# Kernel tuning notes

Hardware: AMD Instinct MI355X
Metric: run time of the kernel (lower is better)

Reference implementation:

```python
import jax, jax.numpy as jnp
import numpy as np

N_HEADS = 8
NODE_DIM, EDGE_DIM, TIME_DIM = 172, 172, 100
OUT_DIM = NODE_DIM + TIME_DIM  # 272, divisible by N_HEADS -> pad_dim = 0
HEAD_DIM = OUT_DIM // N_HEADS  # 34
KEY_DIM = NODE_DIM + EDGE_DIM + TIME_DIM  # 444
B, NBR = 4096, 64
LN_EPS = 1e-5


def setup_inputs() -> dict:
    key = jax.random.key(0)
    ks = jax.random.split(key, 12)
    s = 0.02
    return {
        "node_feat": jax.random.normal(ks[0], (B, NODE_DIM), jnp.float32),
        "time_feat": jax.random.normal(ks[1], (B, 1, TIME_DIM), jnp.float32),
        "edge_feat": jax.random.normal(ks[2], (B, NBR, EDGE_DIM), jnp.float32),
        "nbr_node_feat": jax.random.normal(ks[3], (B, NBR, NODE_DIM), jnp.float32),
        "nbr_time_feat": jax.random.normal(ks[4], (B, NBR, TIME_DIM), jnp.float32),
        "nbr_mask": jax.random.randint(ks[5], (B, NBR), 0, 2, jnp.int32),
        "W_Q": jax.random.normal(ks[6], (OUT_DIM, OUT_DIM), jnp.float32) * s,
        "W_KV": jax.random.normal(ks[7], (2 * OUT_DIM, KEY_DIM), jnp.float32) * s,
        "W_O": jax.random.normal(ks[8], (OUT_DIM, OUT_DIM), jnp.float32) * s,
        "b_O": jax.random.normal(ks[9], (OUT_DIM,), jnp.float32) * s,
        "ln_gamma": jnp.ones((OUT_DIM,), jnp.float32),
        "ln_beta": jnp.zeros((OUT_DIM,), jnp.float32),
    }


def reference(node_feat, time_feat, edge_feat, nbr_node_feat, nbr_time_feat,
              nbr_mask, W_Q, W_KV, W_O, b_O, ln_gamma, ln_beta):
    # Query/residual: concat node + time features -> (B, out_dim) (L=1 squeezed)
    R = jnp.concatenate([node_feat, time_feat[:, 0, :]], axis=-1)  # (B, D)
    Q = R @ W_Q.T  # (B, D)
    # Keys/values from neighbors
    Z_in = jnp.concatenate([nbr_node_feat, edge_feat, nbr_time_feat], axis=-1)  # (B,N,key_dim)
    Z = jnp.einsum('bnk,dk->bnd', Z_in, W_KV)  # (B, N, 2D)
    K, V = Z[..., :OUT_DIM], Z[..., OUT_DIM:]
    # Split heads
    Qh = Q.reshape(B, N_HEADS, HEAD_DIM)              # (B,H,d)
    Kh = K.reshape(B, NBR, N_HEADS, HEAD_DIM)         # (B,N,H,d)
    Vh = V.reshape(B, NBR, N_HEADS, HEAD_DIM)
    # Single-query attention scores: (B,H,N)
    scores = jnp.einsum('bhd,bnhd->bhn', Qh, Kh) * (HEAD_DIM ** -0.5)
    pad = (nbr_mask == 0)[:, None, :]  # (B,1,N)
    scores = jnp.where(pad, jnp.float32(-1e10), scores)
    A = jax.nn.softmax(scores, axis=-1)  # dropout is identity in eval / p=0
    O = jnp.einsum('bhn,bnhd->bhd', A, Vh).reshape(B, OUT_DIM)
    out = O @ W_O.T + b_O
    # Residual + LayerNorm
    x = out + R
    mu = jnp.mean(x, axis=-1, keepdims=True)
    var = jnp.mean(jnp.square(x - mu), axis=-1, keepdims=True)
    return (x - mu) * jax.lax.rsqrt(var + LN_EPS) * ln_gamma + ln_beta
```

## Files before the change

### kernel.cpp

```cpp
#include <hip/hip_runtime.h>
#include <hip/hip_bf16.h>
#include <string.h>

#define NROWS    4096
#define NBR      64
#define NODE_DIM 172
#define EDGE_DIM 172
#define TIME_DIM 100
#define OUT_DIM  272
#define KEY_DIM  444
#define KPAD     448
#define QK_PAD   320
#define N_HEADS  8
#define HEAD_DIM 34

typedef __attribute__((ext_vector_type(8))) short short8_t;
typedef __attribute__((ext_vector_type(4))) float f32x4;

__device__ inline short f2b(float x) {
  unsigned u = __builtin_bit_cast(unsigned, x);
  unsigned r = (u + 0x7fffu + ((u >> 16) & 1u)) >> 16;
  return (short)r;
}

__device__ inline unsigned pk2(float lo, float hi) {
  __hip_bfloat162 h = __float22bfloat162_rn(make_float2(lo, hi));
  unsigned u;
  memcpy(&u, &h, 4);
  return u;
}

template<int ROWS, int KP, int K0>
__device__ inline void pad_rows(char* A, int t) {
  constexpr int NC8 = (KP - K0) / 4;
  constexpr int LPR = 512 / ROWS;
  int r = t / LPR;
  int j = t % LPR;
  char* Arow = A + r * (2 * KP);
  int swz = (r & 7) << 4;
  uint2 zz; zz.x = 0; zz.y = 0;
  for (int c8 = j; c8 < NC8; c8 += LPR)
    *(uint2*)(Arow + ((2 * K0 + 8 * c8) ^ swz)) = zz;
}

template<int MT, int KP, int NKK>
__device__ inline void gemm_tile(const short* __restrict__ Wrow, const char* A,
                                 int lr, int lk, f32x4* acc) {
#pragma unroll
  for (int kk = 0; kk < NKK; ++kk) {
    short8_t bfrag = *(const short8_t*)(Wrow + lr * KP + kk * 32 + lk * 8);
#pragma unroll
    for (int mt = 0; mt < MT; ++mt) {
      short8_t afrag = *(const short8_t*)(A + (mt * 16 + lr) * (2 * KP) +
                                          ((kk * 64 + lk * 16) ^ ((lr & 7) << 4)));
      acc[mt] = __builtin_amdgcn_mfma_f32_16x16x32_bf16(afrag, bfrag, acc[mt], 0, 0, 0);
    }
  }
}

__global__ void convert_w(const float* __restrict__ Wkv, const float* __restrict__ Wq,
                          const float* __restrict__ Wo, short* __restrict__ wq_b,
                          short* __restrict__ wo_b, short* __restrict__ wkt,
                          short* __restrict__ wvh) {
  int i = blockIdx.x * 256 + threadIdx.x;
  if (i < OUT_DIM * QK_PAD) {
    int r = i / QK_PAD, c = i - r * QK_PAD;
    wq_b[i] = (c < OUT_DIM) ? f2b(Wq[r * OUT_DIM + c]) : (short)0;
    wo_b[i] = (c < OUT_DIM) ? f2b(Wo[r * OUT_DIM + c]) : (short)0;
  }
  if (i < N_HEADS * 448 * 64) {
    int h = i / 28672;
    int rem = i - h * 28672;
    int n = rem >> 6, d = rem & 63;
    wkt[i] = (n < KEY_DIM && d < HEAD_DIM) ? f2b(Wkv[(h * HEAD_DIM + d) * KEY_DIM + n])
                                           : (short)0;
  }
  if (i < N_HEADS * 48 * 448) {
    int h = i / 21504;
    int rem = i - h * 21504;
    int cp = rem / 448, k = rem - cp * 448;
    wvh[i] = (cp < HEAD_DIM && k < KEY_DIM)
                 ? f2b(Wkv[(OUT_DIM + h * HEAD_DIM + cp) * KEY_DIM + k])
                 : (short)0;
  }
}

__global__ __launch_bounds__(512) void q_qt(const float* __restrict__ node_feat,
                                            const float* __restrict__ time_feat,
                                            const short* __restrict__ Wq,
                                            const short* __restrict__ Wkt,
                                            short* __restrict__ Qtg) {
  __shared__ char Rlds[16 * 640];
  __shared__ char Qp[16 * 1024];
  int rb = blockIdx.x * 16, t = threadIdx.x;
  {
    int r = t >> 5, j = t & 31;
    const float4* pn = (const float4*)(node_feat + (size_t)(rb + r) * NODE_DIM);
    const float4* pt = (const float4*)(time_feat + (size_t)(rb + r) * TIME_DIM);
    float4 vn[2], vt4;
    int in_[2], it_;
#pragma unroll
    for (int i = 0; i < 2; ++i) { int f = j + 32 * i; in_[i] = f > 42 ? 42 : f; vn[i] = pn[in_[i]]; }
    it_ = j > 24 ? 24 : j; vt4 = pt[it_];
    char* Arow = Rlds + r * 640;
    int swz = (r & 7) << 4;
#pragma unroll
    for (int i = 0; i < 2; ++i) {
      uint2 w; w.x = pk2(vn[i].x, vn[i].y); w.y = pk2(vn[i].z, vn[i].w);
      *(uint2*)(Arow + ((8 * in_[i]) ^ swz)) = w;
    }
    {
      uint2 w; w.x = pk2(vt4.x, vt4.y); w.y = pk2(vt4.z, vt4.w);
      *(uint2*)(Arow + ((344 + 8 * it_) ^ swz)) = w;
    }
    if (j < 12) { uint2 zz; zz.x = 0; zz.y = 0; *(uint2*)(Arow + ((544 + 8 * j) ^ swz)) = zz; }
  }
  {
    uint4 zz; zz.x = 0; zz.y = 0; zz.z = 0; zz.w = 0;
    for (int i = t; i < 1024; i += 512) ((uint4*)Qp)[i] = zz;
  }
  __syncthreads();
  int wave = t >> 6, lane = t & 63, lr = lane & 15, lk = lane >> 4;
  f32x4 z = {0.f, 0.f, 0.f, 0.f};

  for (int nt = wave; nt < 17; nt += 8) {
    int nb = nt * 16;
    f32x4 acc[1] = {z};
    gemm_tile<1, QK_PAD, QK_PAD / 32>(Wq + nb * QK_PAD, Rlds, lr, lk, acc);
    int c = nb + lr;
    int h = c / HEAD_DIM, d = c - h * HEAD_DIM;
#pragma unroll
    for (int e = 0; e < 4; ++e) {
      int r = lk * 4 + e;
      *(short*)(Qp + r * 1024 + h * 128 + ((2 * d) ^ ((r & 7) << 4))) = f2b(acc[0][e]);
    }
  }
  __syncthreads();

  int h = wave;
  const short* Wh = Wkt + h * 28672;
  for (int nt = 0; nt < 28; ++nt) {
    f32x4 acc = z;
#pragma unroll
    for (int kk = 0; kk < 2; ++kk) {
      short8_t bfrag = *(const short8_t*)(Wh + (nt * 16 + lr) * 64 + kk * 32 + lk * 8);
      short8_t afrag = *(const short8_t*)(Qp + lr * 1024 + h * 128 +
                                          ((kk * 64 + lk * 16) ^ ((lr & 7) << 4)));
      acc = __builtin_amdgcn_mfma_f32_16x16x32_bf16(afrag, bfrag, acc, 0, 0, 0);
    }
#pragma unroll
    for (int e = 0; e < 4; ++e)
      Qtg[(size_t)(rb + lk * 4 + e) * 3584 + h * 448 + nt * 16 + lr] =
          f2b(acc[e] * 0.17149858514250882f);
  }
}

__global__ __launch_bounds__(256) void attn5(const float* __restrict__ nbr_node,
                                             const float* __restrict__ edge_feat,
                                             const float* __restrict__ nbr_time,
                                             const int* __restrict__ nbr_mask,
                                             const short* __restrict__ Qtg,
                                             short* __restrict__ Yh2) {
  __shared__ char Zc[32 * 896];
  __shared__ float Spart[2][32][8];
  __shared__ char Pb[16 * 64];
  __shared__ float Mh[8], Lh[8], Fh[8];
  int b = blockIdx.x;
  int t = threadIdx.x;
  int wave = t >> 6, lane = t & 63, lr = lane & 15, lk = lane >> 4;
  f32x4 z = {0.f, 0.f, 0.f, 0.f};
  f32x4 accY[7] = {z, z, z, z, z, z, z};

  for (int ch = 0; ch < 2; ++ch) {
    int n0 = ch * 32;
    {
      int r = t >> 3, j = t & 7;
      const float4* pn = (const float4*)(nbr_node + ((size_t)b * NBR + n0 + r) * NODE_DIM);
      const float4* pe = (const float4*)(edge_feat + ((size_t)b * NBR + n0 + r) * EDGE_DIM);
      const float4* pt = (const float4*)(nbr_time + ((size_t)b * NBR + n0 + r) * TIME_DIM);
      float4 vn[6], ve[6], vt4[4];
      int in_[6], it_[4];
#pragma unroll
      for (int i = 0; i < 6; ++i) { int f = j + 8 * i; in_[i] = f > 42 ? 42 : f; vn[i] = pn[in_[i]]; }
#pragma unroll
      for (int i = 0; i < 6; ++i) ve[i] = pe[in_[i]];
#pragma unroll
      for (int i = 0; i < 4; ++i) { int f = j + 8 * i; it_[i] = f > 24 ? 24 : f; vt4[i] = pt[it_[i]]; }
      char* Arow = Zc + r * 896;
      int swz = (r & 7) << 4;
#pragma unroll
      for (int i = 0; i < 6; ++i) {
        uint2 w; w.x = pk2(vn[i].x, vn[i].y); w.y = pk2(vn[i].z, vn[i].w);
        *(uint2*)(Arow + ((8 * in_[i]) ^ swz)) = w;
      }
#pragma unroll
      for (int i = 0; i < 6; ++i) {
        uint2 w; w.x = pk2(ve[i].x, ve[i].y); w.y = pk2(ve[i].z, ve[i].w);
        *(uint2*)(Arow + ((344 + 8 * in_[i]) ^ swz)) = w;
      }
#pragma unroll
      for (int i = 0; i < 4; ++i) {
        uint2 w; w.x = pk2(vt4[i].x, vt4[i].y); w.y = pk2(vt4[i].z, vt4[i].w);
        *(uint2*)(Arow + ((688 + 8 * it_[i]) ^ swz)) = w;
      }
      if (j == 0) { uint2 zz; zz.x = 0; zz.y = 0; *(uint2*)(Arow + (888 ^ swz)) = zz; }
    }
    __syncthreads();

    {
      int nt = wave & 1, kh = wave >> 1;
      f32x4 acc = z;
      const short* qrow = Qtg + (size_t)b * 3584 + (lr & 7) * 448;
      const char* zbase = Zc + (nt * 16 + lr) * 896;
      int swz = (lr & 7) << 4;
#pragma unroll
      for (int k7 = 0; k7 < 7; ++k7) {
        int ke = (kh * 7 + k7) * 32 + lk * 8;
        short8_t a = *(const short8_t*)(qrow + ke);
        short8_t bb = *(const short8_t*)(zbase + ((2 * ke) ^ swz));
        acc = __builtin_amdgcn_mfma_f32_16x16x32_bf16(a, bb, acc, 0, 0, 0);
      }
#pragma unroll
      for (int e = 0; e < 4; ++e) {
        int h = lk * 4 + e;
        if (h < 8) Spart[kh][nt * 16 + lr][h] = acc[e];
      }
    }
    __syncthreads();

    {
      int h = wave * 2 + (lane >> 5);
      int n = lane & 31;
      float s = Spart[0][n][h] + Spart[1][n][h];
      if (nbr_mask[(size_t)b * NBR + n0 + n] == 0) s = -1e10f;
      float m = s;
#pragma unroll
      for (int off = 16; off >= 1; off >>= 1) m = fmaxf(m, __shfl_xor(m, off));
      float mp = (ch == 0) ? -3e38f : Mh[h];
      float mn = fmaxf(mp, m);
      float e = __expf(s - mn);
      float sum = e;
#pragma unroll
      for (int off = 16; off >= 1; off >>= 1) sum += __shfl_xor(sum, off);
      float f = __expf(mp - mn);
      if (n == 0) {
        Lh[h] = (ch == 0 ? 0.f : Lh[h]) * f + sum;
        Mh[h] = mn;
        Fh[h] = f;
      }
      int off2 = (2 * n) ^ ((h & 3) << 4);
      *(short*)(Pb + h * 64 + off2) = f2b(e);
      *(short*)(Pb + (h + 8) * 64 + off2) = 0;
    }
    __syncthreads();

    {
      short8_t pa = *(const short8_t*)(Pb + lr * 64 + ((lk * 16) ^ ((lr & 3) << 4)));
      const char* zb_base = Zc + (lk * 8) * 896;
#pragma unroll
      for (int s7 = 0; s7 < 7; ++s7) {
        int vt = wave + 4 * s7;
#pragma unroll
        for (int e = 0; e < 4; ++e) accY[s7][e] *= Fh[(lk * 4 + e) & 7];
        int colb = 2 * (vt * 16 + lr);
        short8_t zb;
#pragma unroll
        for (int jx = 0; jx < 8; ++jx)
          zb[jx] = *(const short*)(zb_base + jx * 896 + (colb ^ (jx << 4)));
        accY[s7] = __builtin_amdgcn_mfma_f32_16x16x32_bf16(pa, zb, accY[s7], 0, 0, 0);
      }
    }
    __syncthreads();
  }

  if (lk < 2) {
    float inv[4];
#pragma unroll
    for (int e = 0; e < 4; ++e) inv[e] = 1.f / Lh[lk * 4 + e];
#pragma unroll
    for (int s7 = 0; s7 < 7; ++s7) {
      int vt = wave + 4 * s7;
      int k = vt * 16 + lr, kk2 = k >> 5, kp = k & 31;
#pragma unroll
      for (int e = 0; e < 4; ++e)
        Yh2[((size_t)((lk * 4 + e) * 14 + kk2) * 4096 + b) * 32 + kp] =
            f2b(accY[s7][e] * inv[e]);
    }
  }
}

__global__ __launch_bounds__(512) void out_ln2(const short* __restrict__ Yh2,
                                               const short* __restrict__ Wvh,
                                               const short* __restrict__ Wo,
                                               const float* __restrict__ bO,
                                               const float* __restrict__ node_feat,
                                               const float* __restrict__ time_feat,
                                               const float* __restrict__ gamma,
                                               const float* __restrict__ beta,
                                               float* __restrict__ out) {
  __shared__ char Alds[16 * 640];
  __shared__ float X[16 * 276];
  int rb = blockIdx.x * 16;
  int t = threadIdx.x;
  int wave = t >> 6, lane = t & 63, lr = lane & 15, lk = lane >> 4;
  pad_rows<16, QK_PAD, OUT_DIM>(Alds, t);
  f32x4 z = {0.f, 0.f, 0.f, 0.f};

  for (int p = wave; p < 24; p += 8) {
    int h = p / 3, nt = p - h * 3;
    f32x4 acc = z;
#pragma unroll
    for (int kk = 0; kk < 14; ++kk) {
      short8_t bfrag = *(const short8_t*)(Wvh + h * 21504 + (nt * 16 + lr) * 448 +
                                          kk * 32 + lk * 8);
      short8_t afrag = *(const short8_t*)(
          Yh2 + ((size_t)(h * 14 + kk) * 4096 + rb + lr) * 32 + lk * 8);
      acc = __builtin_amdgcn_mfma_f32_16x16x32_bf16(afrag, bfrag, acc, 0, 0, 0);
    }
    int cl = nt * 16 + lr;
    if (cl < HEAD_DIM) {
      int c = h * HEAD_DIM + cl;
#pragma unroll
      for (int e = 0; e < 4; ++e) {
        int r = lk * 4 + e;
        *(short*)(Alds + r * 640 + ((2 * c) ^ ((r & 7) << 4))) = f2b(acc[e]);
      }
    }
  }
  __syncthreads();

  for (int nt = wave; nt < 17; nt += 8) {
    int nb = nt * 16;
    f32x4 acc[1] = {z};
    gemm_tile<1, QK_PAD, QK_PAD / 32>(Wo + nb * QK_PAD, Alds, lr, lk, acc);
    int c = nb + lr;
    float bo = bO[c];
#pragma unroll
    for (int e = 0; e < 4; ++e) {
      int r = lk * 4 + e;
      int gr = rb + r;
      float Rv = (c < NODE_DIM) ? node_feat[(size_t)gr * NODE_DIM + c]
                                : time_feat[(size_t)gr * TIME_DIM + (c - NODE_DIM)];
      X[r * 276 + c] = acc[0][e] + bo + Rv;
    }
  }
  __syncthreads();

  int row = t >> 5, j = t & 31;
  float s1 = 0.f, s2 = 0.f;
  for (int c = j; c < OUT_DIM; c += 32) {
    float v = X[row * 276 + c];
    s1 += v; s2 += v * v;
  }
#pragma unroll
  for (int off = 16; off >= 1; off >>= 1) {
    s1 += __shfl_xor(s1, off);
    s2 += __shfl_xor(s2, off);
  }
  float mu = s1 * (1.f / OUT_DIM);
  float var = s2 * (1.f / OUT_DIM) - mu * mu;
  float inv = rsqrtf(fmaxf(var, 0.f) + 1e-5f);
  int gr = rb + row;
  for (int c = j; c < OUT_DIM; c += 32) {
    float v = X[row * 276 + c];
    out[(size_t)gr * OUT_DIM + c] = (v - mu) * inv * gamma[c] + beta[c];
  }
}

extern "C" void kernel_launch(void* const* d_in, const int* in_sizes, int n_in,
                              void* d_out, int out_size, void* d_ws, size_t ws_size,
                              hipStream_t stream) {
  const float* node_feat = (const float*)d_in[0];
  const float* time_feat = (const float*)d_in[1];
  const float* edge_feat = (const float*)d_in[2];
  const float* nbr_node  = (const float*)d_in[3];
  const float* nbr_time  = (const float*)d_in[4];
  const int*   nbr_mask  = (const int*)d_in[5];
  const float* W_Q   = (const float*)d_in[6];
  const float* W_KV  = (const float*)d_in[7];
  const float* W_O   = (const float*)d_in[8];
  const float* b_O   = (const float*)d_in[9];
  const float* gamma = (const float*)d_in[10];
  const float* beta  = (const float*)d_in[11];
  float* out = (float*)d_out;
  char* ws = (char*)d_ws;

  short* wq_b = (short*)(ws);
  short* wo_b = (short*)(ws + 174080);
  short* wvh  = (short*)(ws + 348160);
  short* wkt  = (short*)(ws + 692224);
  short* Qtg  = (short*)(ws + 1150976);
  short* Yh2  = (short*)(ws + 30511104);

  convert_w<<<896, 256, 0, stream>>>(W_KV, W_Q, W_O, wq_b, wo_b, wkt, wvh);
  q_qt<<<NROWS / 16, 512, 0, stream>>>(node_feat, time_feat, wq_b, wkt, Qtg);
  attn5<<<NROWS, 256, 0, stream>>>(nbr_node, edge_feat, nbr_time, nbr_mask, Qtg, Yh2);
  out_ln2<<<NROWS / 16, 512, 0, stream>>>(Yh2, wvh, wo_b, b_O, node_feat, time_feat,
                                          gamma, beta, out);
}
```

Before: 202.9 us.

## Double-buffer neighbor features via async global-to-LDS loads in persistent attention blocks

The attention kernel now runs 256 blocks of 512 threads, each processing 16 batch rows in 32 half-chunks. It uses global_load_lds to prefetch the next chunk's raw fp32 neighbor, edge and time rows into a second LDS buffer while the current one is computed. The fp32-to-bf16 conversion moves from staging into the MFMA operand fetch. The key dimension is re-padded per segment (480), so weight layouts, Qt and Yh2 strides change throughout the pipeline. The aim is to hide global load latency and remove register staging. The cost is doubled LDS (about 120KB per block), one resident block per CU, and repeated conversion work in the score and value passes.

```diff
diff --git a/kernel.cpp b/kernel.cpp
--- a/kernel.cpp
+++ b/kernel.cpp
@@ -9,13 +9,14 @@
 #define TIME_DIM 100
 #define OUT_DIM  272
 #define KEY_DIM  444
-#define KPAD     448
 #define QK_PAD   320
 #define N_HEADS  8
 #define HEAD_DIM 34
+#define KP3      480
 
 typedef __attribute__((ext_vector_type(8))) short short8_t;
 typedef __attribute__((ext_vector_type(4))) float f32x4;
+typedef __attribute__((ext_vector_type(4))) unsigned uintx4;
 
 __device__ inline short f2b(float x) {
   unsigned u = __builtin_bit_cast(unsigned, x);
@@ -28,6 +29,12 @@
   unsigned u;
   memcpy(&u, &h, 4);
   return u;
+}
+
+typedef const __attribute__((address_space(1))) void gv_t;
+typedef __attribute__((address_space(3))) void lv_t;
+__device__ inline void gld16(const void* g, void* l) {
+  __builtin_amdgcn_global_load_lds((gv_t*)g, (lv_t*)l, 16, 0, 0);
 }
 
 template<int ROWS, int KP, int K0>
@@ -58,6 +65,12 @@
   }
 }
 
+__device__ inline int kmap(int kp, bool& valid) {
+  if (kp < 176) { valid = kp < 172; return kp; }
+  if (kp < 352) { valid = kp < 348; return kp - 4; }
+  valid = kp < 452; return kp - 8;
+}
+
 __global__ void convert_w(const float* __restrict__ Wkv, const float* __restrict__ Wq,
                           const float* __restrict__ Wo, short* __restrict__ wq_b,
                           short* __restrict__ wo_b, short* __restrict__ wkt,
@@ -68,19 +81,20 @@
     wq_b[i] = (c < OUT_DIM) ? f2b(Wq[r * OUT_DIM + c]) : (short)0;
     wo_b[i] = (c < OUT_DIM) ? f2b(Wo[r * OUT_DIM + c]) : (short)0;
   }
-  if (i < N_HEADS * 448 * 64) {
-    int h = i / 28672;
-    int rem = i - h * 28672;
-    int n = rem >> 6, d = rem & 63;
-    wkt[i] = (n < KEY_DIM && d < HEAD_DIM) ? f2b(Wkv[(h * HEAD_DIM + d) * KEY_DIM + n])
-                                           : (short)0;
-  }
-  if (i < N_HEADS * 48 * 448) {
-    int h = i / 21504;
-    int rem = i - h * 21504;
-    int cp = rem / 448, k = rem - cp * 448;
-    wvh[i] = (cp < HEAD_DIM && k < KEY_DIM)
-                 ? f2b(Wkv[(OUT_DIM + h * HEAD_DIM + cp) * KEY_DIM + k])
+  if (i < N_HEADS * KP3 * 64) {
+    int h = i / (KP3 * 64);
+    int rem = i - h * (KP3 * 64);
+    int np = rem >> 6, d = rem & 63;
+    bool v; int kn = kmap(np, v);
+    wkt[i] = (v && d < HEAD_DIM) ? f2b(Wkv[(h * HEAD_DIM + d) * KEY_DIM + kn]) : (short)0;
+  }
+  if (i < N_HEADS * 48 * KP3) {
+    int h = i / (48 * KP3);
+    int rem = i - h * (48 * KP3);
+    int cp = rem / KP3, kp = rem - cp * KP3;
+    bool v; int kn = kmap(kp, v);
+    wvh[i] = (v && cp < HEAD_DIM)
+                 ? f2b(Wkv[(OUT_DIM + h * HEAD_DIM + cp) * KEY_DIM + kn])
                  : (short)0;
   }
 }
@@ -138,8 +152,8 @@
   __syncthreads();
 
   int h = wave;
-  const short* Wh = Wkt + h * 28672;
-  for (int nt = 0; nt < 28; ++nt) {
+  const short* Wh = Wkt + h * (KP3 * 64);
+  for (int nt = 0; nt < 30; ++nt) {
     f32x4 acc = z;
 #pragma unroll
     for (int kk = 0; kk < 2; ++kk) {
@@ -150,101 +164,114 @@
     }
 #pragma unroll
     for (int e = 0; e < 4; ++e)
-      Qtg[(size_t)(rb + lk * 4 + e) * 3584 + h * 448 + nt * 16 + lr] =
+      Qtg[(size_t)(rb + lk * 4 + e) * (8 * KP3) + h * KP3 + nt * 16 + lr] =
           f2b(acc[e] * 0.17149858514250882f);
   }
 }
 
-__global__ __launch_bounds__(256) void attn5(const float* __restrict__ nbr_node,
+__device__ inline void stage_issue(const float* __restrict__ nn,
+                                   const float* __restrict__ ef,
+                                   const float* __restrict__ tf,
+                                   int b, int half, char* buf, int wave, int lane) {
+  size_t rowbase = (size_t)b * NBR + half * 32;
+  for (int q = wave; q < 22; q += 8) {
+    int F = q * 1024 + lane * 16;
+    int row = (int)((unsigned)F / 704u);
+    int col = F - row * 704;
+    col = col > 672 ? 672 : col;
+    gld16((const char*)nn + (rowbase + row) * 688 + col, buf + q * 1024);
+  }
+  for (int q = wave; q < 22; q += 8) {
+    int F = q * 1024 + lane * 16;
+    int row = (int)((unsigned)F / 704u);
+    int col = F - row * 704;
+    col = col > 672 ? 672 : col;
+    gld16((const char*)ef + (rowbase + row) * 688 + col, buf + 22528 + q * 1024);
+  }
+  for (int q = wave; q < 16; q += 8) {
+    int F = q * 1024 + lane * 16;
+    int row = F >> 9;
+    int col = F & 511;
+    col = col > 384 ? 384 : col;
+    gld16((const char*)tf + (rowbase + row) * 400 + col, buf + 45056 + q * 1024);
+  }
+}
+
+__global__ __launch_bounds__(512) void attn6(const float* __restrict__ nbr_node,
                                              const float* __restrict__ edge_feat,
                                              const float* __restrict__ nbr_time,
                                              const int* __restrict__ nbr_mask,
                                              const short* __restrict__ Qtg,
                                              short* __restrict__ Yh2) {
-  __shared__ char Zc[32 * 896];
-  __shared__ float Spart[2][32][8];
+  __shared__ char Zb[2][61440];
+  __shared__ float Spart[4][32][8];
   __shared__ char Pb[16 * 64];
   __shared__ float Mh[8], Lh[8], Fh[8];
-  int b = blockIdx.x;
   int t = threadIdx.x;
   int wave = t >> 6, lane = t & 63, lr = lane & 15, lk = lane >> 4;
   f32x4 z = {0.f, 0.f, 0.f, 0.f};
-  f32x4 accY[7] = {z, z, z, z, z, z, z};
-
-  for (int ch = 0; ch < 2; ++ch) {
-    int n0 = ch * 32;
+  f32x4 accY[4] = {z, z, z, z};
+  int bbase = blockIdx.x * 16;
+
+  stage_issue(nbr_node, edge_feat, nbr_time, bbase, 0, Zb[0], wave, lane);
+  __syncthreads();
+
+  for (int ci = 0; ci < 32; ++ci) {
+    int b = bbase + (ci >> 1);
+    int half = ci & 1;
+    char* cur = Zb[ci & 1];
+    if (ci + 1 < 32)
+      stage_issue(nbr_node, edge_feat, nbr_time, bbase + ((ci + 1) >> 1), (ci + 1) & 1,
+                  Zb[(ci + 1) & 1], wave, lane);
+
     {
-      int r = t >> 3, j = t & 7;
-      const float4* pn = (const float4*)(nbr_node + ((size_t)b * NBR + n0 + r) * NODE_DIM);
-      const float4* pe = (const float4*)(edge_feat + ((size_t)b * NBR + n0 + r) * EDGE_DIM);
-      const float4* pt = (const float4*)(nbr_time + ((size_t)b * NBR + n0 + r) * TIME_DIM);
-      float4 vn[6], ve[6], vt4[4];
-      int in_[6], it_[4];
-#pragma unroll
-      for (int i = 0; i < 6; ++i) { int f = j + 8 * i; in_[i] = f > 42 ? 42 : f; vn[i] = pn[in_[i]]; }
-#pragma unroll
-      for (int i = 0; i < 6; ++i) ve[i] = pe[in_[i]];
-#pragma unroll
-      for (int i = 0; i < 4; ++i) { int f = j + 8 * i; it_[i] = f > 24 ? 24 : f; vt4[i] = pt[it_[i]]; }
-      char* Arow = Zc + r * 896;
-      int swz = (r & 7) << 4;
-#pragma unroll
-      for (int i = 0; i < 6; ++i) {
-        uint2 w; w.x = pk2(vn[i].x, vn[i].y); w.y = pk2(vn[i].z, vn[i].w);
-        *(uint2*)(Arow + ((8 * in_[i]) ^ swz)) = w;
-      }
-#pragma unroll
-      for (int i = 0; i < 6; ++i) {
-        uint2 w; w.x = pk2(ve[i].x, ve[i].y); w.y = pk2(ve[i].z, ve[i].w);
-        *(uint2*)(Arow + ((344 + 8 * in_[i]) ^ swz)) = w;
-      }
-#pragma unroll
-      for (int i = 0; i < 4; ++i) {
-        uint2 w; w.x = pk2(vt4[i].x, vt4[i].y); w.y = pk2(vt4[i].z, vt4[i].w);
-        *(uint2*)(Arow + ((688 + 8 * it_[i]) ^ swz)) = w;
-      }
-      if (j == 0) { uint2 zz; zz.x = 0; zz.y = 0; *(uint2*)(Arow + (888 ^ swz)) = zz; }
-    }
-    __syncthreads();
-
-    {
-      int nt = wave & 1, kh = wave >> 1;
+      int ntl = wave & 1, kh = wave >> 1;
       f32x4 acc = z;
-      const short* qrow = Qtg + (size_t)b * 3584 + (lr & 7) * 448;
-      const char* zbase = Zc + (nt * 16 + lr) * 896;
-      int swz = (lr & 7) << 4;
-#pragma unroll
-      for (int k7 = 0; k7 < 7; ++k7) {
-        int ke = (kh * 7 + k7) * 32 + lk * 8;
-        short8_t a = *(const short8_t*)(qrow + ke);
-        short8_t bb = *(const short8_t*)(zbase + ((2 * ke) ^ swz));
-        acc = __builtin_amdgcn_mfma_f32_16x16x32_bf16(a, bb, acc, 0, 0, 0);
+      const short* qrow = Qtg + (size_t)b * (8 * KP3) + (lr & 7) * KP3;
+      int r = ntl * 16 + lr;
+#pragma unroll
+      for (int k7 = 0; k7 < 4; ++k7) {
+        int kt = kh * 4 + k7;
+        if (kt < 15) {
+          int ke = kt * 32 + lk * 8;
+          const char* zrow; int cb;
+          if (ke < 176)      { zrow = cur + r * 704;         cb = 4 * ke; }
+          else if (ke < 352) { zrow = cur + 22528 + r * 704; cb = 4 * (ke - 176); }
+          else               { zrow = cur + 45056 + r * 512; cb = 4 * (ke - 352); }
+          float4 f0 = *(const float4*)(zrow + cb);
+          float4 f1 = *(const float4*)(zrow + cb + 16);
+          uintx4 pk;
+          pk[0] = pk2(f0.x, f0.y); pk[1] = pk2(f0.z, f0.w);
+          pk[2] = pk2(f1.x, f1.y); pk[3] = pk2(f1.z, f1.w);
+          short8_t bb = __builtin_bit_cast(short8_t, pk);
+          short8_t a = *(const short8_t*)(qrow + ke);
+          acc = __builtin_amdgcn_mfma_f32_16x16x32_bf16(a, bb, acc, 0, 0, 0);
+        }
       }
 #pragma unroll
       for (int e = 0; e < 4; ++e) {
         int h = lk * 4 + e;
-        if (h < 8) Spart[kh][nt * 16 + lr][h] = acc[e];
+        if (h < 8) Spart[kh][ntl * 16 + lr][h] = acc[e];
       }
     }
     __syncthreads();
 
     {
-      int h = wave * 2 + (lane >> 5);
-      int n = lane & 31;
-      float s = Spart[0][n][h] + Spart[1][n][h];
-      if (nbr_mask[(size_t)b * NBR + n0 + n] == 0) s = -1e10f;
+      int h = wave, n = lane & 31;
+      float s = Spart[0][n][h] + Spart[1][n][h] + Spart[2][n][h] + Spart[3][n][h];
+      if (nbr_mask[(size_t)b * NBR + half * 32 + n] == 0) s = -1e10f;
       float m = s;
 #pragma unroll
       for (int off = 16; off >= 1; off >>= 1) m = fmaxf(m, __shfl_xor(m, off));
-      float mp = (ch == 0) ? -3e38f : Mh[h];
+      float mp = (half == 0) ? -3e38f : Mh[h];
       float mn = fmaxf(mp, m);
       float e = __expf(s - mn);
       float sum = e;
 #pragma unroll
       for (int off = 16; off >= 1; off >>= 1) sum += __shfl_xor(sum, off);
       float f = __expf(mp - mn);
-      if (n == 0) {
-        Lh[h] = (ch == 0 ? 0.f : Lh[h]) * f + sum;
+      if (lane == 0) {
+        Lh[h] = (half ? Lh[h] : 0.f) * f + sum;
         Mh[h] = mn;
         Fh[h] = f;
       }
@@ -256,36 +283,51 @@
 
     {
       short8_t pa = *(const short8_t*)(Pb + lr * 64 + ((lk * 16) ^ ((lr & 3) << 4)));
-      const char* zb_base = Zc + (lk * 8) * 896;
-#pragma unroll
-      for (int s7 = 0; s7 < 7; ++s7) {
-        int vt = wave + 4 * s7;
-#pragma unroll
-        for (int e = 0; e < 4; ++e) accY[s7][e] *= Fh[(lk * 4 + e) & 7];
-        int colb = 2 * (vt * 16 + lr);
-        short8_t zb;
-#pragma unroll
-        for (int jx = 0; jx < 8; ++jx)
-          zb[jx] = *(const short*)(zb_base + jx * 896 + (colb ^ (jx << 4)));
-        accY[s7] = __builtin_amdgcn_mfma_f32_16x16x32_bf16(pa, zb, accY[s7], 0, 0, 0);
+#pragma unroll
+      for (int s7 = 0; s7 < 4; ++s7) {
+        int vt = wave + 8 * s7;
+        if (vt < 30) {
+          int kcol = vt * 16 + lr;
+          const char* zc; int strd;
+          if (kcol < 176)      { zc = cur + (lk * 8) * 704 + 4 * kcol;                strd = 704; }
+          else if (kcol < 352) { zc = cur + 22528 + (lk * 8) * 704 + 4 * (kcol - 176); strd = 704; }
+          else                 { zc = cur + 45056 + (lk * 8) * 512 + 4 * (kcol - 352); strd = 512; }
+          float zf0 = *(const float*)(zc);
+          float zf1 = *(const float*)(zc + strd);
+          float zf2 = *(const float*)(zc + 2 * strd);
+          float zf3 = *(const float*)(zc + 3 * strd);
+          float zf4 = *(const float*)(zc + 4 * strd);
+          float zf5 = *(const float*)(zc + 5 * strd);
+          float zf6 = *(const float*)(zc + 6 * strd);
+          float zf7 = *(const float*)(zc + 7 * strd);
+          uintx4 pk;
+          pk[0] = pk2(zf0, zf1); pk[1] = pk2(zf2, zf3);
+          pk[2] = pk2(zf4, zf5); pk[3] = pk2(zf6, zf7);
+          short8_t zb = __builtin_bit_cast(short8_t, pk);
+#pragma unroll
+          for (int e = 0; e < 4; ++e) accY[s7][e] *= Fh[(lk * 4 + e) & 7];
+          accY[s7] = __builtin_amdgcn_mfma_f32_16x16x32_bf16(pa, zb, accY[s7], 0, 0, 0);
+        }
+      }
+    }
+
+    if (half == 1 && lk < 2) {
+      float inv[4];
+#pragma unroll
+      for (int e = 0; e < 4; ++e) inv[e] = 1.f / Lh[lk * 4 + e];
+#pragma unroll
+      for (int s7 = 0; s7 < 4; ++s7) {
+        int vt = wave + 8 * s7;
+        if (vt < 30) {
+          int k = vt * 16 + lr, kk2 = k >> 5, kp = k & 31;
+#pragma unroll
+          for (int e = 0; e < 4; ++e)
+            Yh2[((size_t)((lk * 4 + e) * 15 + kk2) * 4096 + b) * 32 + kp] =
+                f2b(accY[s7][e] * inv[e]);
+        }
       }
     }
     __syncthreads();
-  }
-
-  if (lk < 2) {
-    float inv[4];
-#pragma unroll
-    for (int e = 0; e < 4; ++e) inv[e] = 1.f / Lh[lk * 4 + e];
-#pragma unroll
-    for (int s7 = 0; s7 < 7; ++s7) {
-      int vt = wave + 4 * s7;
-      int k = vt * 16 + lr, kk2 = k >> 5, kp = k & 31;
-#pragma unroll
-      for (int e = 0; e < 4; ++e)
-        Yh2[((size_t)((lk * 4 + e) * 14 + kk2) * 4096 + b) * 32 + kp] =
-            f2b(accY[s7][e] * inv[e]);
-    }
   }
 }
 
@@ -310,11 +352,11 @@
     int h = p / 3, nt = p - h * 3;
     f32x4 acc = z;
 #pragma unroll
-    for (int kk = 0; kk < 14; ++kk) {
-      short8_t bfrag = *(const short8_t*)(Wvh + h * 21504 + (nt * 16 + lr) * 448 +
+    for (int kk = 0; kk < 15; ++kk) {
+      short8_t bfrag = *(const short8_t*)(Wvh + h * (48 * KP3) + (nt * 16 + lr) * KP3 +
                                           kk * 32 + lk * 8);
       short8_t afrag = *(const short8_t*)(
-          Yh2 + ((size_t)(h * 14 + kk) * 4096 + rb + lr) * 32 + lk * 8);
+          Yh2 + ((size_t)(h * 15 + kk) * 4096 + rb + lr) * 32 + lk * 8);
       acc = __builtin_amdgcn_mfma_f32_16x16x32_bf16(afrag, bfrag, acc, 0, 0, 0);
     }
     int cl = nt * 16 + lr;
@@ -388,13 +430,13 @@
   short* wq_b = (short*)(ws);
   short* wo_b = (short*)(ws + 174080);
   short* wvh  = (short*)(ws + 348160);
-  short* wkt  = (short*)(ws + 692224);
-  short* Qtg  = (short*)(ws + 1150976);
-  short* Yh2  = (short*)(ws + 30511104);
-
-  convert_w<<<896, 256, 0, stream>>>(W_KV, W_Q, W_O, wq_b, wo_b, wkt, wvh);
+  short* wkt  = (short*)(ws + 716800);
+  short* Qtg  = (short*)(ws + 1208320);
+  short* Yh2  = (short*)(ws + 32665600);
+
+  convert_w<<<960, 256, 0, stream>>>(W_KV, W_Q, W_O, wq_b, wo_b, wkt, wvh);
   q_qt<<<NROWS / 16, 512, 0, stream>>>(node_feat, time_feat, wq_b, wkt, Qtg);
-  attn5<<<NROWS, 256, 0, stream>>>(nbr_node, edge_feat, nbr_time, nbr_mask, Qtg, Yh2);
+  attn6<<<256, 512, 0, stream>>>(nbr_node, edge_feat, nbr_time, nbr_mask, Qtg, Yh2);
   out_ln2<<<NROWS / 16, 512, 0, stream>>>(Yh2, wvh, wo_b, b_O, node_feat, time_feat,
                                           gamma, beta, out);
 }
```

Measured after the change: 223.1 us. 1.1x slower.

## Process all 64 neighbors in one pass with 512-thread attention blocks

Applied to the files above, without the earlier changes.

Replaces the two-chunk online-softmax attention kernel with a single pass. One 512-thread block stages all 64 neighbor rows in LDS, then computes scores, a plain softmax and the P·Z product. It also prefetches the Q fragments and the mask into registers before the feature load. This removes the per-chunk rescaling and several barriers, but doubles LDS use to about 57KB per block, which may limit how many blocks fit on each CU.

```diff
diff --git a/kernel.cpp b/kernel.cpp
--- a/kernel.cpp
+++ b/kernel.cpp
@@ -155,136 +155,120 @@
   }
 }
 
-__global__ __launch_bounds__(256) void attn5(const float* __restrict__ nbr_node,
+__global__ __launch_bounds__(512) void attn3(const float* __restrict__ nbr_node,
                                              const float* __restrict__ edge_feat,
                                              const float* __restrict__ nbr_time,
                                              const int* __restrict__ nbr_mask,
                                              const short* __restrict__ Qtg,
                                              short* __restrict__ Yh2) {
-  __shared__ char Zc[32 * 896];
-  __shared__ float Spart[2][32][8];
-  __shared__ char Pb[16 * 64];
-  __shared__ float Mh[8], Lh[8], Fh[8];
+  __shared__ char Alds[64 * 896];
+  __shared__ float Spart[2][64][8];
+  __shared__ char Pb[16 * 128];
   int b = blockIdx.x;
   int t = threadIdx.x;
   int wave = t >> 6, lane = t & 63, lr = lane & 15, lk = lane >> 4;
+
+  int ntw = wave & 3, kh = wave >> 2;
+  const short* qrow = Qtg + (size_t)b * 3584 + (lr & 7) * 448;
+  short8_t qpre[7];
+#pragma unroll
+  for (int k7 = 0; k7 < 7; ++k7)
+    qpre[k7] = *(const short8_t*)(qrow + (kh * 7 + k7) * 32 + lk * 8);
+  int mpre = nbr_mask[(size_t)b * NBR + lane];
+
+  {
+    int r = t >> 3, j = t & 7;
+    const float4* pn = (const float4*)(nbr_node + (size_t)b * NBR * NODE_DIM) + (size_t)r * 43;
+    const float4* pe = (const float4*)(edge_feat + (size_t)b * NBR * EDGE_DIM) + (size_t)r * 43;
+    const float4* pt = (const float4*)(nbr_time + (size_t)b * NBR * TIME_DIM) + (size_t)r * 25;
+    float4 vn[6], ve[6], vt4[4];
+    int in_[6], it_[4];
+#pragma unroll
+    for (int i = 0; i < 6; ++i) { int f = j + 8 * i; in_[i] = f > 42 ? 42 : f; vn[i] = pn[in_[i]]; }
+#pragma unroll
+    for (int i = 0; i < 6; ++i) { ve[i] = pe[in_[i]]; }
+#pragma unroll
+    for (int i = 0; i < 4; ++i) { int f = j + 8 * i; it_[i] = f > 24 ? 24 : f; vt4[i] = pt[it_[i]]; }
+    char* Arow = Alds + r * 896;
+    int swz = (r & 7) << 4;
+#pragma unroll
+    for (int i = 0; i < 6; ++i) {
+      uint2 w; w.x = pk2(vn[i].x, vn[i].y); w.y = pk2(vn[i].z, vn[i].w);
+      *(uint2*)(Arow + ((8 * in_[i]) ^ swz)) = w;
+    }
+#pragma unroll
+    for (int i = 0; i < 6; ++i) {
+      uint2 w; w.x = pk2(ve[i].x, ve[i].y); w.y = pk2(ve[i].z, ve[i].w);
+      *(uint2*)(Arow + ((344 + 8 * in_[i]) ^ swz)) = w;
+    }
+#pragma unroll
+    for (int i = 0; i < 4; ++i) {
+      uint2 w; w.x = pk2(vt4[i].x, vt4[i].y); w.y = pk2(vt4[i].z, vt4[i].w);
+      *(uint2*)(Arow + ((688 + 8 * it_[i]) ^ swz)) = w;
+    }
+    if (j == 0) { uint2 zz; zz.x = 0; zz.y = 0; *(uint2*)(Arow + (888 ^ swz)) = zz; }
+  }
+  __syncthreads();
+
   f32x4 z = {0.f, 0.f, 0.f, 0.f};
-  f32x4 accY[7] = {z, z, z, z, z, z, z};
-
-  for (int ch = 0; ch < 2; ++ch) {
-    int n0 = ch * 32;
-    {
-      int r = t >> 3, j = t & 7;
-      const float4* pn = (const float4*)(nbr_node + ((size_t)b * NBR + n0 + r) * NODE_DIM);
-      const float4* pe = (const float4*)(edge_feat + ((size_t)b * NBR + n0 + r) * EDGE_DIM);
-      const float4* pt = (const float4*)(nbr_time + ((size_t)b * NBR + n0 + r) * TIME_DIM);
-      float4 vn[6], ve[6], vt4[4];
-      int in_[6], it_[4];
-#pragma unroll
-      for (int i = 0; i < 6; ++i) { int f = j + 8 * i; in_[i] = f > 42 ? 42 : f; vn[i] = pn[in_[i]]; }
-#pragma unroll
-      for (int i = 0; i < 6; ++i) ve[i] = pe[in_[i]];
-#pragma unroll
-      for (int i = 0; i < 4; ++i) { int f = j + 8 * i; it_[i] = f > 24 ? 24 : f; vt4[i] = pt[it_[i]]; }
-      char* Arow = Zc + r * 896;
-      int swz = (r & 7) << 4;
-#pragma unroll
-      for (int i = 0; i < 6; ++i) {
-        uint2 w; w.x = pk2(vn[i].x, vn[i].y); w.y = pk2(vn[i].z, vn[i].w);
-        *(uint2*)(Arow + ((8 * in_[i]) ^ swz)) = w;
-      }
-#pragma unroll
-      for (int i = 0; i < 6; ++i) {
-        uint2 w; w.x = pk2(ve[i].x, ve[i].y); w.y = pk2(ve[i].z, ve[i].w);
-        *(uint2*)(Arow + ((344 + 8 * in_[i]) ^ swz)) = w;
-      }
-#pragma unroll
-      for (int i = 0; i < 4; ++i) {
-        uint2 w; w.x = pk2(vt4[i].x, vt4[i].y); w.y = pk2(vt4[i].z, vt4[i].w);
-        *(uint2*)(Arow + ((688 + 8 * it_[i]) ^ swz)) = w;
-      }
-      if (j == 0) { uint2 zz; zz.x = 0; zz.y = 0; *(uint2*)(Arow + (888 ^ swz)) = zz; }
-    }
-    __syncthreads();
-
-    {
-      int nt = wave & 1, kh = wave >> 1;
-      f32x4 acc = z;
-      const short* qrow = Qtg + (size_t)b * 3584 + (lr & 7) * 448;
-      const char* zbase = Zc + (nt * 16 + lr) * 896;
-      int swz = (lr & 7) << 4;
-#pragma unroll
-      for (int k7 = 0; k7 < 7; ++k7) {
-        int ke = (kh * 7 + k7) * 32 + lk * 8;
-        short8_t a = *(const short8_t*)(qrow + ke);
-        short8_t bb = *(const short8_t*)(zbase + ((2 * ke) ^ swz));
-        acc = __builtin_amdgcn_mfma_f32_16x16x32_bf16(a, bb, acc, 0, 0, 0);
-      }
+
+  {
+    f32x4 acc = z;
+    const char* zbase = Alds + (ntw * 16 + lr) * 896;
+    int swz = (lr & 7) << 4;
+#pragma unroll
+    for (int k7 = 0; k7 < 7; ++k7) {
+      int ke = (kh * 7 + k7) * 32 + lk * 8;
+      short8_t bbv = *(const short8_t*)(zbase + ((2 * ke) ^ swz));
+      acc = __builtin_amdgcn_mfma_f32_16x16x32_bf16(qpre[k7], bbv, acc, 0, 0, 0);
+    }
+#pragma unroll
+    for (int e = 0; e < 4; ++e) {
+      int h = lk * 4 + e;
+      if (h < 8) Spart[kh][ntw * 16 + lr][h] = acc[e];
+    }
+  }
+  __syncthreads();
+
+  {
+    int h = wave, n = lane;
+    float s = Spart[0][n][h] + Spart[1][n][h];
+    if (mpre == 0) s = -1e10f;
+    float m = s;
+#pragma unroll
+    for (int off = 32; off >= 1; off >>= 1) m = fmaxf(m, __shfl_xor(m, off));
+    float e = __expf(s - m);
+    float sum = e;
+#pragma unroll
+    for (int off = 32; off >= 1; off >>= 1) sum += __shfl_xor(sum, off);
+    int off2 = (2 * n) ^ ((h & 7) << 4);
+    *(short*)(Pb + h * 128 + off2) = f2b(e / sum);
+    *(short*)(Pb + (h + 8) * 128 + off2) = 0;
+  }
+  __syncthreads();
+
+  for (int vt = wave; vt < 28; vt += 8) {
+    int vb = vt * 16;
+    f32x4 acc = z;
+    int colb = 2 * (vb + lr);
+#pragma unroll
+    for (int kk = 0; kk < 2; ++kk) {
+      short8_t pa = *(const short8_t*)(Pb + lr * 128 +
+                                       ((kk * 64 + lk * 16) ^ ((lr & 7) << 4)));
+      const char* zb_base = Alds + (kk * 32 + lk * 8) * 896;
+      short8_t zb;
+#pragma unroll
+      for (int j = 0; j < 8; ++j)
+        zb[j] = *(const short*)(zb_base + j * 896 + (colb ^ (j << 4)));
+      acc = __builtin_amdgcn_mfma_f32_16x16x32_bf16(pa, zb, acc, 0, 0, 0);
+    }
+    if (lk < 2) {
+      int k = vb + lr, kk2 = k >> 5, kp = k & 31;
 #pragma unroll
       for (int e = 0; e < 4; ++e) {
         int h = lk * 4 + e;
-        if (h < 8) Spart[kh][nt * 16 + lr][h] = acc[e];
+        Yh2[((size_t)(h * 14 + kk2) * 4096 + b) * 32 + kp] = f2b(acc[e]);
       }
-    }
-    __syncthreads();
-
-    {
-      int h = wave * 2 + (lane >> 5);
-      int n = lane & 31;
-      float s = Spart[0][n][h] + Spart[1][n][h];
-      if (nbr_mask[(size_t)b * NBR + n0 + n] == 0) s = -1e10f;
-      float m = s;
-#pragma unroll
-      for (int off = 16; off >= 1; off >>= 1) m = fmaxf(m, __shfl_xor(m, off));
-      float mp = (ch == 0) ? -3e38f : Mh[h];
-      float mn = fmaxf(mp, m);
-      float e = __expf(s - mn);
-      float sum = e;
-#pragma unroll
-      for (int off = 16; off >= 1; off >>= 1) sum += __shfl_xor(sum, off);
-      float f = __expf(mp - mn);
-      if (n == 0) {
-        Lh[h] = (ch == 0 ? 0.f : Lh[h]) * f + sum;
-        Mh[h] = mn;
-        Fh[h] = f;
-      }
-      int off2 = (2 * n) ^ ((h & 3) << 4);
-      *(short*)(Pb + h * 64 + off2) = f2b(e);
-      *(short*)(Pb + (h + 8) * 64 + off2) = 0;
-    }
-    __syncthreads();
-
-    {
-      short8_t pa = *(const short8_t*)(Pb + lr * 64 + ((lk * 16) ^ ((lr & 3) << 4)));
-      const char* zb_base = Zc + (lk * 8) * 896;
-#pragma unroll
-      for (int s7 = 0; s7 < 7; ++s7) {
-        int vt = wave + 4 * s7;
-#pragma unroll
-        for (int e = 0; e < 4; ++e) accY[s7][e] *= Fh[(lk * 4 + e) & 7];
-        int colb = 2 * (vt * 16 + lr);
-        short8_t zb;
-#pragma unroll
-        for (int jx = 0; jx < 8; ++jx)
-          zb[jx] = *(const short*)(zb_base + jx * 896 + (colb ^ (jx << 4)));
-        accY[s7] = __builtin_amdgcn_mfma_f32_16x16x32_bf16(pa, zb, accY[s7], 0, 0, 0);
-      }
-    }
-    __syncthreads();
-  }
-
-  if (lk < 2) {
-    float inv[4];
-#pragma unroll
-    for (int e = 0; e < 4; ++e) inv[e] = 1.f / Lh[lk * 4 + e];
-#pragma unroll
-    for (int s7 = 0; s7 < 7; ++s7) {
-      int vt = wave + 4 * s7;
-      int k = vt * 16 + lr, kk2 = k >> 5, kp = k & 31;
-#pragma unroll
-      for (int e = 0; e < 4; ++e)
-        Yh2[((size_t)((lk * 4 + e) * 14 + kk2) * 4096 + b) * 32 + kp] =
-            f2b(accY[s7][e] * inv[e]);
     }
   }
 }
@@ -394,7 +378,7 @@
 
   convert_w<<<896, 256, 0, stream>>>(W_KV, W_Q, W_O, wq_b, wo_b, wkt, wvh);
   q_qt<<<NROWS / 16, 512, 0, stream>>>(node_feat, time_feat, wq_b, wkt, Qtg);
-  attn5<<<NROWS, 256, 0, stream>>>(nbr_node, edge_feat, nbr_time, nbr_mask, Qtg, Yh2);
+  attn3<<<NROWS, 512, 0, stream>>>(nbr_node, edge_feat, nbr_time, nbr_mask, Qtg, Yh2);
   out_ln2<<<NROWS / 16, 512, 0, stream>>>(Yh2, wvh, wo_b, b_O, node_feat, time_feat,
                                           gamma, beta, out);
 }
```

New measurement: 170.3 us. 1.19x faster.

## Make attention kernel persistent with double-buffered async global-to-LDS neighbor loads

Applied to the files above, without the earlier changes.

Replaces the one-block-per-row attention kernel with a 512-thread block that loops over 16 rows in 32-neighbor chunks. The next chunk's fp32 neighbor features and the precomputed Qt row are prefetched directly into LDS with global_load_lds while the current chunk is converted and processed. The Qt layout is also changed to a swizzled form so it can be staged into LDS. This aims to hide global memory latency and cut per-block launch overhead. The cost is a large LDS footprint (about 130KB), which limits occupancy to roughly one block per CU, and only 256 blocks are launched.

```diff
diff --git a/kernel.cpp b/kernel.cpp
--- a/kernel.cpp
+++ b/kernel.cpp
@@ -28,6 +28,18 @@
   unsigned u;
   memcpy(&u, &h, 4);
   return u;
+}
+
+typedef const __attribute__((address_space(1))) void gv_t;
+typedef __attribute__((address_space(3))) void lv_t;
+__device__ inline void gld16(const void* g, void* l) {
+  __builtin_amdgcn_global_load_lds((gv_t*)g, (lv_t*)l, 16, 0, 0);
+}
+
+__device__ inline void barrier_lgkm() {
+  asm volatile("s_waitcnt lgkmcnt(0)" ::: "memory");
+  __builtin_amdgcn_sched_barrier(0);
+  __builtin_amdgcn_s_barrier();
 }
 
 template<int ROWS, int KP, int K0>
@@ -149,102 +161,142 @@
       acc = __builtin_amdgcn_mfma_f32_16x16x32_bf16(afrag, bfrag, acc, 0, 0, 0);
     }
 #pragma unroll
-    for (int e = 0; e < 4; ++e)
-      Qtg[(size_t)(rb + lk * 4 + e) * 3584 + h * 448 + nt * 16 + lr] =
-          f2b(acc[e] * 0.17149858514250882f);
-  }
-}
-
-__global__ __launch_bounds__(256) void attn5(const float* __restrict__ nbr_node,
-                                             const float* __restrict__ edge_feat,
-                                             const float* __restrict__ nbr_time,
+    for (int e = 0; e < 4; ++e) {
+      int n = nt * 16 + lr;
+      *(short*)((char*)Qtg + (size_t)(rb + lk * 4 + e) * 7168 + h * 896 +
+                ((2 * n) ^ (h << 4))) = f2b(acc[e] * 0.17149858514250882f);
+    }
+  }
+}
+
+__device__ inline void stage_chunk(const float* __restrict__ nn,
+                                   const float* __restrict__ ef,
+                                   const float* __restrict__ tf,
+                                   const short* __restrict__ Qtg,
+                                   int b, int half, char* buf, char* qtslot, char* dump,
+                                   int wave, int lane) {
+  size_t row0 = (size_t)b * NBR + half * 32;
+  const char* nb = (const char*)(nn + row0 * NODE_DIM);
+  const char* eb = (const char*)(ef + row0 * EDGE_DIM);
+  const char* tb = (const char*)(tf + row0 * TIME_DIM);
+  const char* qb = (const char*)Qtg + (size_t)b * 7168;
+#pragma unroll
+  for (int i = 0; i < 8; ++i) {
+    int q = wave * 8 + i;
+    if (q < 22) {
+      int off = q * 1024 + lane * 16; if (off > 22000) off = 22000;
+      gld16(nb + off, buf + q * 1024);
+    } else if (q < 44) {
+      int off = (q - 22) * 1024 + lane * 16; if (off > 22000) off = 22000;
+      gld16(eb + off, buf + 22528 + (q - 22) * 1024);
+    } else if (q < 57) {
+      int off = (q - 44) * 1024 + lane * 16; if (off > 12784) off = 12784;
+      gld16(tb + off, buf + 45056 + (q - 44) * 1024);
+    } else {
+      int off = (q - 57) * 1024 + lane * 16;
+      gld16(qb + off, half == 0 ? (qtslot + (q - 57) * 1024) : dump);
+    }
+  }
+}
+
+__global__ __launch_bounds__(512) void attn7(const float* __restrict__ nn,
+                                             const float* __restrict__ ef,
+                                             const float* __restrict__ tf,
                                              const int* __restrict__ nbr_mask,
                                              const short* __restrict__ Qtg,
                                              short* __restrict__ Yh2) {
-  __shared__ char Zc[32 * 896];
-  __shared__ float Spart[2][32][8];
+  __shared__ char Zbuf[2][58368];
+  __shared__ char QtS[2][7168];
+  __shared__ char Dump[1024];
+  __shared__ float Spart[4][32][8];
   __shared__ char Pb[16 * 64];
   __shared__ float Mh[8], Lh[8], Fh[8];
-  int b = blockIdx.x;
+  __shared__ int Mlds[1024];
   int t = threadIdx.x;
   int wave = t >> 6, lane = t & 63, lr = lane & 15, lk = lane >> 4;
+  int bbase = blockIdx.x * 16;
   f32x4 z = {0.f, 0.f, 0.f, 0.f};
-  f32x4 accY[7] = {z, z, z, z, z, z, z};
-
-  for (int ch = 0; ch < 2; ++ch) {
-    int n0 = ch * 32;
+  f32x4 accY[4] = {z, z, z, z};
+
+  if (t < 256) ((int4*)Mlds)[t] = ((const int4*)(nbr_mask + (size_t)bbase * 64))[t];
+  stage_chunk(nn, ef, tf, Qtg, bbase, 0, Zbuf[0], QtS[0], Dump, wave, lane);
+
+  for (int ci = 0; ci < 32; ++ci) {
+    int b = bbase + (ci >> 1), half = ci & 1;
+    char* cur = Zbuf[ci & 1];
+
+    if (ci < 31) {
+      int b2 = bbase + ((ci + 1) >> 1);
+      stage_chunk(nn, ef, tf, Qtg, b2, (ci + 1) & 1, Zbuf[(ci + 1) & 1], QtS[b2 & 1],
+                  Dump, wave, lane);
+      asm volatile("s_waitcnt vmcnt(8) lgkmcnt(0)" ::: "memory");
+    } else {
+      asm volatile("s_waitcnt vmcnt(0) lgkmcnt(0)" ::: "memory");
+    }
+    __builtin_amdgcn_sched_barrier(0);
+    __builtin_amdgcn_s_barrier();
+
+    int r = t >> 4, j = t & 15;
+    f32x4 v[7];
+#pragma unroll
+    for (int i = 0; i < 7; ++i) {
+      int k = j * 4 + i * 64;
+      int off = (k < 172) ? (r * 688 + 4 * k)
+              : (k < 344) ? (22528 + r * 688 + 4 * (k - 172))
+                          : (45056 + r * 400 + 4 * (k - 344));
+      v[i] = *(const f32x4*)(cur + off);
+    }
+    if (j == 15) { v[6][0] = 0.f; v[6][1] = 0.f; v[6][2] = 0.f; v[6][3] = 0.f; }
+    barrier_lgkm();
     {
-      int r = t >> 3, j = t & 7;
-      const float4* pn = (const float4*)(nbr_node + ((size_t)b * NBR + n0 + r) * NODE_DIM);
-      const float4* pe = (const float4*)(edge_feat + ((size_t)b * NBR + n0 + r) * EDGE_DIM);
-      const float4* pt = (const float4*)(nbr_time + ((size_t)b * NBR + n0 + r) * TIME_DIM);
-      float4 vn[6], ve[6], vt4[4];
-      int in_[6], it_[4];
-#pragma unroll
-      for (int i = 0; i < 6; ++i) { int f = j + 8 * i; in_[i] = f > 42 ? 42 : f; vn[i] = pn[in_[i]]; }
-#pragma unroll
-      for (int i = 0; i < 6; ++i) ve[i] = pe[in_[i]];
-#pragma unroll
-      for (int i = 0; i < 4; ++i) { int f = j + 8 * i; it_[i] = f > 24 ? 24 : f; vt4[i] = pt[it_[i]]; }
-      char* Arow = Zc + r * 896;
+      char* Arow = cur + r * 896;
       int swz = (r & 7) << 4;
 #pragma unroll
-      for (int i = 0; i < 6; ++i) {
-        uint2 w; w.x = pk2(vn[i].x, vn[i].y); w.y = pk2(vn[i].z, vn[i].w);
-        *(uint2*)(Arow + ((8 * in_[i]) ^ swz)) = w;
-      }
-#pragma unroll
-      for (int i = 0; i < 6; ++i) {
-        uint2 w; w.x = pk2(ve[i].x, ve[i].y); w.y = pk2(ve[i].z, ve[i].w);
-        *(uint2*)(Arow + ((344 + 8 * in_[i]) ^ swz)) = w;
-      }
-#pragma unroll
-      for (int i = 0; i < 4; ++i) {
-        uint2 w; w.x = pk2(vt4[i].x, vt4[i].y); w.y = pk2(vt4[i].z, vt4[i].w);
-        *(uint2*)(Arow + ((688 + 8 * it_[i]) ^ swz)) = w;
-      }
-      if (j == 0) { uint2 zz; zz.x = 0; zz.y = 0; *(uint2*)(Arow + (888 ^ swz)) = zz; }
-    }
-    __syncthreads();
+      for (int i = 0; i < 7; ++i) {
+        uint2 w; w.x = pk2(v[i][0], v[i][1]); w.y = pk2(v[i][2], v[i][3]);
+        *(uint2*)(Arow + ((8 * j + 128 * i) ^ swz)) = w;
+      }
+    }
+    barrier_lgkm();
 
     {
-      int nt = wave & 1, kh = wave >> 1;
+      int ntl = wave & 1, kq = wave >> 1;
+      int tb0 = kq < 2 ? kq * 4 : 8 + (kq - 2) * 3;
+      int cnt = kq < 2 ? 4 : 3;
       f32x4 acc = z;
-      const short* qrow = Qtg + (size_t)b * 3584 + (lr & 7) * 448;
-      const char* zbase = Zc + (nt * 16 + lr) * 896;
+      const char* qbase = QtS[b & 1] + (lr & 7) * 896;
+      const char* zbase = cur + (ntl * 16 + lr) * 896;
       int swz = (lr & 7) << 4;
-#pragma unroll
-      for (int k7 = 0; k7 < 7; ++k7) {
-        int ke = (kh * 7 + k7) * 32 + lk * 8;
-        short8_t a = *(const short8_t*)(qrow + ke);
-        short8_t bb = *(const short8_t*)(zbase + ((2 * ke) ^ swz));
+      for (int it = 0; it < cnt; ++it) {
+        int keb = 2 * ((tb0 + it) * 32 + lk * 8);
+        short8_t a = *(const short8_t*)(qbase + (keb ^ swz));
+        short8_t bb = *(const short8_t*)(zbase + (keb ^ swz));
         acc = __builtin_amdgcn_mfma_f32_16x16x32_bf16(a, bb, acc, 0, 0, 0);
       }
 #pragma unroll
       for (int e = 0; e < 4; ++e) {
         int h = lk * 4 + e;
-        if (h < 8) Spart[kh][nt * 16 + lr][h] = acc[e];
-      }
-    }
-    __syncthreads();
+        if (h < 8) Spart[kq][ntl * 16 + lr][h] = acc[e];
+      }
+    }
+    barrier_lgkm();
 
     {
-      int h = wave * 2 + (lane >> 5);
-      int n = lane & 31;
-      float s = Spart[0][n][h] + Spart[1][n][h];
-      if (nbr_mask[(size_t)b * NBR + n0 + n] == 0) s = -1e10f;
+      int h = wave, n = lane & 31;
+      float s = Spart[0][n][h] + Spart[1][n][h] + Spart[2][n][h] + Spart[3][n][h];
+      if (Mlds[(ci >> 1) * 64 + half * 32 + n] == 0) s = -1e10f;
       float m = s;
 #pragma unroll
       for (int off = 16; off >= 1; off >>= 1) m = fmaxf(m, __shfl_xor(m, off));
-      float mp = (ch == 0) ? -3e38f : Mh[h];
+      float mp = (half == 0) ? -3e38f : Mh[h];
       float mn = fmaxf(mp, m);
       float e = __expf(s - mn);
       float sum = e;
 #pragma unroll
       for (int off = 16; off >= 1; off >>= 1) sum += __shfl_xor(sum, off);
       float f = __expf(mp - mn);
-      if (n == 0) {
-        Lh[h] = (ch == 0 ? 0.f : Lh[h]) * f + sum;
+      if (lane == 0) {
+        Lh[h] = (half ? Lh[h] : 0.f) * f + sum;
         Mh[h] = mn;
         Fh[h] = f;
       }
@@ -252,40 +304,43 @@
       *(short*)(Pb + h * 64 + off2) = f2b(e);
       *(short*)(Pb + (h + 8) * 64 + off2) = 0;
     }
-    __syncthreads();
+    barrier_lgkm();
 
     {
       short8_t pa = *(const short8_t*)(Pb + lr * 64 + ((lk * 16) ^ ((lr & 3) << 4)));
-      const char* zb_base = Zc + (lk * 8) * 896;
-#pragma unroll
-      for (int s7 = 0; s7 < 7; ++s7) {
-        int vt = wave + 4 * s7;
-#pragma unroll
-        for (int e = 0; e < 4; ++e) accY[s7][e] *= Fh[(lk * 4 + e) & 7];
-        int colb = 2 * (vt * 16 + lr);
-        short8_t zb;
-#pragma unroll
-        for (int jx = 0; jx < 8; ++jx)
-          zb[jx] = *(const short*)(zb_base + jx * 896 + (colb ^ (jx << 4)));
-        accY[s7] = __builtin_amdgcn_mfma_f32_16x16x32_bf16(pa, zb, accY[s7], 0, 0, 0);
-      }
-    }
-    __syncthreads();
-  }
-
-  if (lk < 2) {
-    float inv[4];
-#pragma unroll
-    for (int e = 0; e < 4; ++e) inv[e] = 1.f / Lh[lk * 4 + e];
-#pragma unroll
-    for (int s7 = 0; s7 < 7; ++s7) {
-      int vt = wave + 4 * s7;
-      int k = vt * 16 + lr, kk2 = k >> 5, kp = k & 31;
-#pragma unroll
-      for (int e = 0; e < 4; ++e)
-        Yh2[((size_t)((lk * 4 + e) * 14 + kk2) * 4096 + b) * 32 + kp] =
-            f2b(accY[s7][e] * inv[e]);
-    }
+#pragma unroll
+      for (int s7 = 0; s7 < 4; ++s7) {
+        int vt = wave + 8 * s7;
+        if (vt < 28) {
+          int colb = 2 * (vt * 16 + lr);
+          const char* zb_base = cur + (lk * 8) * 896;
+          short8_t zb;
+#pragma unroll
+          for (int jx = 0; jx < 8; ++jx)
+            zb[jx] = *(const short*)(zb_base + jx * 896 + (colb ^ (jx << 4)));
+#pragma unroll
+          for (int e = 0; e < 4; ++e) accY[s7][e] *= Fh[(lk * 4 + e) & 7];
+          accY[s7] = __builtin_amdgcn_mfma_f32_16x16x32_bf16(pa, zb, accY[s7], 0, 0, 0);
+        }
+      }
+      if (half == 1 && lk < 2) {
+        float inv[4];
+#pragma unroll
+        for (int e = 0; e < 4; ++e) inv[e] = 1.f / Lh[lk * 4 + e];
+#pragma unroll
+        for (int s7 = 0; s7 < 4; ++s7) {
+          int vt = wave + 8 * s7;
+          if (vt < 28) {
+            int k = vt * 16 + lr, kk2 = k >> 5, kp = k & 31;
+#pragma unroll
+            for (int e = 0; e < 4; ++e)
+              Yh2[((size_t)((lk * 4 + e) * 14 + kk2) * 4096 + b) * 32 + kp] =
+                  f2b(accY[s7][e] * inv[e]);
+          }
+        }
+      }
+    }
+    __builtin_amdgcn_s_barrier();
   }
 }
 
@@ -394,7 +449,7 @@
 
   convert_w<<<896, 256, 0, stream>>>(W_KV, W_Q, W_O, wq_b, wo_b, wkt, wvh);
   q_qt<<<NROWS / 16, 512, 0, stream>>>(node_feat, time_feat, wq_b, wkt, Qtg);
-  attn5<<<NROWS, 256, 0, stream>>>(nbr_node, edge_feat, nbr_time, nbr_mask, Qtg, Yh2);
+  attn7<<<256, 512, 0, stream>>>(nbr_node, edge_feat, nbr_time, nbr_mask, Qtg, Yh2);
   out_ln2<<<NROWS / 16, 512, 0, stream>>>(Yh2, wvh, wo_b, b_O, node_feat, time_feat,
                                           gamma, beta, out);
 }
```

After: 198.8 us. -2.0%, faster.
